# Kernel optimization log

Hardware: AMD Instinct MI355X
Metric: run time of the kernel (lower is better)

## Reference

```python
import jax, jax.numpy as jnp
import numpy as np

B, M, N = 2, 256, 256
K, P, Q, D = 8, 512, 512, 64
R, Pp, Qp, Dp = 128, 512, 512, 64
TEMP = float(np.sqrt(Dp))  # softmax temperature = sqrt(D')


def _xavier(key, shape):
    # xavier_uniform over last two dims (fan_in, fan_out), matching torch init on (K, d, D)
    fan_in, fan_out = shape[-2], shape[-1]
    lim = float(np.sqrt(6.0 / (fan_in + fan_out)))
    return jax.random.uniform(key, shape, jnp.float32, -lim, lim)


def setup_inputs() -> dict:
    key = jax.random.key(0)
    ks = jax.random.split(key, 9)
    return {
        "z": jax.random.normal(ks[0], (B, M, N, R), jnp.float32),
        "y_q": jax.random.normal(ks[1], (B, N, Qp), jnp.float32),
        "x_k": jax.random.normal(ks[2], (B, M, Pp), jnp.float32),
        "Theta_x": _xavier(ks[3], (K, P, D)),
        "Theta_y": _xavier(ks[4], (K, Q, D)),
        "Lam_x": _xavier(ks[5], (K, Pp, Dp)),
        "Lam_y": _xavier(ks[6], (K, Qp, Dp)),
        "Lam_zx": _xavier(ks[7], (K, R, Dp)),
        "Lam_zy": _xavier(ks[8], (K, R, Dp)),
    }


def reference(z, y_q, x_k, Theta_x, Theta_y, Lam_x, Lam_y, Lam_zx, Lam_zy):
    # --- mixed attention scores ---
    xt = jnp.einsum('bmp,kpd->bkmd', x_k, Lam_x)          # [B,K,M,D']
    yt = jnp.einsum('bnq,kqd->bknd', y_q, Lam_y)          # [B,K,N,D']
    r = jnp.einsum('bkmd,bknd->bkmn', xt, yt)             # pairwise term
    zy = jnp.einsum('bmnr,krd->bkmnd', z, Lam_zy)         # [B,K,M,N,D'] (large)
    r = r + jnp.einsum('bkmnd,bkmd->bkmn', zy, xt)
    r = r + jnp.einsum('bknd,bmnr,krd->bkmn', yt, z, Lam_zx)
    # --- generalised convolution (mask=None, bias=False) ---
    a = jax.nn.softmax(r / TEMP, axis=-2)                 # softmax over M (column-wise)
    xv = jnp.einsum('bmp,kpd->bkmd', x_k, Theta_x)        # value projection
    y = jnp.einsum('bkmn,bkmd,kqd->bnq', a, xv, Theta_y)  # [B,N,Q]
    return y
```

## Files before the change

kernel.cpp:

```cpp
#include <hip/hip_runtime.h>
#include <hip/hip_bf16.h>

#define LOG2E_OVER_T 0.18033688011112042f

typedef __attribute__((ext_vector_type(8))) short short8;
typedef __attribute__((ext_vector_type(4))) float f32x4;
typedef unsigned short ushort_t;
typedef unsigned long long ull_t;

#define MFMA16(a, b, c) __builtin_amdgcn_mfma_f32_16x16x32_bf16(a, b, c, 0, 0, 0)

__device__ __forceinline__ ushort_t f2bf(float f) {
    union { float f; unsigned u; } v; v.f = f;
    unsigned r = (v.u + 0x7fffu + ((v.u >> 16) & 1u)) >> 16;
    return (ushort_t)r;
}

__device__ __forceinline__ void mfma_core64(
    const ushort_t* __restrict__ Ag, int lda,
    const ushort_t* __restrict__ Btg, int ldb,
    int ksteps, f32x4 acc[2][2])
{
    __shared__ __align__(16) ushort_t As[64 * 40];
    __shared__ __align__(16) ushort_t Bs[64 * 40];
    const int t = threadIdx.x;
    const int srow = t >> 2, skc = (t & 3) * 8;
    const int lane = t & 63, w = t >> 6;
    const int wr = w >> 1, wc = w & 1;
    const int fr = lane & 15, kg = lane >> 4;
    const int aoff = (wr * 32 + fr) * 40 + kg * 8;
    const int boff = (wc * 32 + fr) * 40 + kg * 8;
    const long arow = (long)srow * lda + skc;
    const long brow = (long)srow * ldb + skc;

    short8 ra = *(const short8*)(Ag + arow);
    short8 rb = *(const short8*)(Btg + brow);
    for (int kt = 0; kt < ksteps; kt++) {
        __syncthreads();
        *(short8*)&As[srow * 40 + skc] = ra;
        *(short8*)&Bs[srow * 40 + skc] = rb;
        __syncthreads();
        if (kt + 1 < ksteps) {
            ra = *(const short8*)(Ag + arow + (kt + 1) * 32);
            rb = *(const short8*)(Btg + brow + (kt + 1) * 32);
        }
        short8 a0 = *(const short8*)&As[aoff];
        short8 a1 = *(const short8*)&As[aoff + 16 * 40];
        short8 b0 = *(const short8*)&Bs[boff];
        short8 b1 = *(const short8*)&Bs[boff + 16 * 40];
        acc[0][0] = MFMA16(a0, b0, acc[0][0]);
        acc[0][1] = MFMA16(a0, b1, acc[0][1]);
        acc[1][0] = MFMA16(a1, b0, acc[1][0]);
        acc[1][1] = MFMA16(a1, b1, acc[1][1]);
    }
}

__device__ __forceinline__ void zero_acc(f32x4 acc[2][2]) {
    const f32x4 z4 = {0.f, 0.f, 0.f, 0.f};
    acc[0][0] = z4; acc[0][1] = z4; acc[1][0] = z4; acc[1][1] = z4;
}

__global__ __launch_bounds__(256)
void convert_kernel(const float* __restrict__ x_k, const float* __restrict__ y_q,
                    const float* __restrict__ Lam_x, const float* __restrict__ Theta_x,
                    const float* __restrict__ Lam_y, const float* __restrict__ Lam_zy,
                    const float* __restrict__ Lam_zx, const float* __restrict__ Theta_y,
                    ushort_t* __restrict__ xkb, ushort_t* __restrict__ yqb,
                    ushort_t* __restrict__ WxTb, ushort_t* __restrict__ WyTb,
                    ushort_t* __restrict__ Zyb, ushort_t* __restrict__ Zxb,
                    ushort_t* __restrict__ TyTb)
{
    int i = blockIdx.x * 256 + threadIdx.x;
    if (i < 262144) { xkb[i] = f2bf(x_k[i]); return; }
    i -= 262144;
    if (i < 262144) { yqb[i] = f2bf(y_q[i]); return; }
    i -= 262144;
    if (i < 524288) {
        const int k = i >> 16, rem = i & 65535, dc = rem >> 9, p = i & 511;
        const float v = (dc < 64) ? Lam_x[((long)k * 512 + p) * 64 + dc]
                                  : Theta_x[((long)k * 512 + p) * 64 + dc - 64];
        WxTb[i] = f2bf(v); return;
    }
    i -= 524288;
    if (i < 262144) {
        const int k = i >> 15, d = (i >> 9) & 63, p = i & 511;
        WyTb[i] = f2bf(Lam_y[((long)k * 512 + p) * 64 + d]); return;
    }
    i -= 262144;
    if (i < 65536) { Zyb[i] = f2bf(Lam_zy[i]); return; }
    i -= 65536;
    if (i < 65536) { Zxb[i] = f2bf(Lam_zx[i]); return; }
    i -= 65536;
    {
        const int q = i >> 9, kd = i & 511, k = kd >> 6, d = kd & 63;
        TyTb[i] = f2bf(Theta_y[((long)k * 512 + q) * 64 + d]);
    }
}

__global__ __launch_bounds__(256)
void proj_kernel(const ushort_t* __restrict__ xkb, const ushort_t* __restrict__ yqb,
                 const ushort_t* __restrict__ WxTb, const ushort_t* __restrict__ WyTb,
                 ushort_t* __restrict__ xtb, ushort_t* __restrict__ ytb,
                 ushort_t* __restrict__ xvTb)
{
    const int side = blockIdx.z;
    const int bx = blockIdx.x, by = blockIdx.y;
    if (side == 1 && bx >= 8) return;
    f32x4 acc[2][2]; zero_acc(acc);
    const int t = threadIdx.x, lane = t & 63, w = t >> 6;
    const int wr = w >> 1, wc = w & 1, fr = lane & 15, kg = lane >> 4;

    if (side == 0) {
        mfma_core64(xkb + (long)(by * 64) * 512, 512,
                    WxTb + (long)(bx * 64) * 512, 512, 16, acc);
        const int k = bx >> 1, isxv = bx & 1;
        #pragma unroll
        for (int mi = 0; mi < 2; mi++)
        #pragma unroll
        for (int ni = 0; ni < 2; ni++) {
            const int grow0 = by * 64 + wr * 32 + mi * 16 + kg * 4;
            const int b = grow0 >> 8, m0 = grow0 & 255;
            const int d = wc * 32 + ni * 16 + fr;
            if (!isxv) {
                #pragma unroll
                for (int j = 0; j < 4; j++)
                    xtb[(((long)(b * 8 + k)) * 256 + m0 + j) * 64 + d] = f2bf(acc[mi][ni][j]);
            } else {
                ull_t pk = (ull_t)f2bf(acc[mi][ni][0])
                         | ((ull_t)f2bf(acc[mi][ni][1]) << 16)
                         | ((ull_t)f2bf(acc[mi][ni][2]) << 32)
                         | ((ull_t)f2bf(acc[mi][ni][3]) << 48);
                *(ull_t*)&xvTb[(((long)(b * 8 + k)) * 64 + d) * 256 + m0] = pk;
            }
        }
    } else {
        mfma_core64(yqb + (long)(by * 64) * 512, 512,
                    WyTb + (long)(bx * 64) * 512, 512, 16, acc);
        const int k = bx;
        #pragma unroll
        for (int mi = 0; mi < 2; mi++)
        #pragma unroll
        for (int ni = 0; ni < 2; ni++)
        #pragma unroll
        for (int j = 0; j < 4; j++) {
            const int grow = by * 64 + wr * 32 + mi * 16 + kg * 4 + j;
            const int b = grow >> 8, n = grow & 255;
            const int d = wc * 32 + ni * 16 + fr;
            ytb[(((long)(b * 8 + k)) * 256 + n) * 64 + d] = f2bf(acc[mi][ni][j]);
        }
    }
}

__global__ __launch_bounds__(256)
void step2_kernel(const ushort_t* __restrict__ xtb, const ushort_t* __restrict__ ytb,
                  const ushort_t* __restrict__ Zyb, const ushort_t* __restrict__ Zxb,
                  float* __restrict__ wzy, float* __restrict__ wzx,
                  float* __restrict__ rbuf)
{
    const int bz = blockIdx.x;
    const ushort_t *Ag, *Btg;
    float* C; int ldc; long coff;
    if (bz < 256) {
        const int which = bz >> 7, idx = bz & 127;
        const int bk = idx >> 3, tile = idx & 7, mt = tile >> 1, nt = tile & 1;
        const int k = bk & 7;
        Ag = (which ? ytb : xtb) + ((long)bk * 256 + mt * 64) * 64;
        Btg = (which ? Zxb : Zyb) + ((long)k * 128 + nt * 64) * 64;
        C = which ? wzx : wzy; ldc = 128;
        coff = ((long)bk * 256 + mt * 64) * 128 + nt * 64;
    } else {
        const int idx = bz - 256;
        const int bk = idx >> 4, tile = idx & 15, mt = tile >> 2, nt = tile & 3;
        Ag = xtb + ((long)bk * 256 + mt * 64) * 64;
        Btg = ytb + ((long)bk * 256 + nt * 64) * 64;
        C = rbuf; ldc = 256;
        coff = ((long)bk * 256 + mt * 64) * 256 + nt * 64;
    }
    f32x4 acc[2][2]; zero_acc(acc);
    mfma_core64(Ag, 64, Btg, 64, 2, acc);
    const int t = threadIdx.x, lane = t & 63, w = t >> 6;
    const int wr = w >> 1, wc = w & 1, fr = lane & 15, kg = lane >> 4;
    #pragma unroll
    for (int mi = 0; mi < 2; mi++)
    #pragma unroll
    for (int ni = 0; ni < 2; ni++)
    #pragma unroll
    for (int j = 0; j < 4; j++)
        C[coff + (long)(wr * 32 + mi * 16 + kg * 4 + j) * ldc + wc * 32 + ni * 16 + fr]
            = acc[mi][ni][j];
}

__global__ __launch_bounds__(256)
void pass1_kernel(const float* __restrict__ z, const float* __restrict__ wzy,
                  float* __restrict__ rbuf)
{
    const int m = blockIdx.x, b = blockIdx.y;
    __shared__ __align__(16) float zs[64 * 128];
    __shared__ __align__(16) float ws[8 * 128];
    const int tid = threadIdx.x;
    {
        const int k = tid >> 5, r4 = tid & 31;
        *(float4*)&ws[k * 128 + r4 * 4] =
            *(const float4*)&wzy[(((long)b * 8 + k) * 256 + m) * 128 + r4 * 4];
    }
    const int k = tid >> 5, nl = tid & 31;
    const int sw = nl & 7;
    __syncthreads();
    for (int n0 = 0; n0 < 256; n0 += 64) {
        if (n0) __syncthreads();
        const float4* zg = (const float4*)(z + (((long)b * 256 + m) * 256 + n0) * 128);
        #pragma unroll
        for (int it = 0; it < 8; it++) {
            const int idx = it * 256 + tid;
            const int nn = idx >> 5, r4 = idx & 31;
            ((float4*)zs)[nn * 32 + (r4 ^ (nn & 7))] = zg[idx];
        }
        __syncthreads();
        float acc0 = 0.f, acc1 = 0.f;
        #pragma unroll 4
        for (int r4 = 0; r4 < 32; r4++) {
            const float4 wv = ((const float4*)ws)[k * 32 + r4];
            const float4 z0 = ((const float4*)zs)[nl * 32 + (r4 ^ sw)];
            const float4 z1 = ((const float4*)zs)[(nl + 32) * 32 + (r4 ^ sw)];
            acc0 += z0.x * wv.x + z0.y * wv.y + z0.z * wv.z + z0.w * wv.w;
            acc1 += z1.x * wv.x + z1.y * wv.y + z1.z * wv.z + z1.w * wv.w;
        }
        float* rp = rbuf + (((long)b * 8 + k) * 256 + m) * 256 + n0 + nl;
        rp[0]  += acc0;
        rp[32] += acc1;
    }
}

__global__ __launch_bounds__(256)
void pass2_kernel(const float* __restrict__ z, const float* __restrict__ wzx,
                  float* __restrict__ rbufT)
{
    const int n = blockIdx.x, b = blockIdx.y;
    __shared__ __align__(16) float zs[64 * 128];
    __shared__ __align__(16) float ws[8 * 128];
    const int tid = threadIdx.x;
    {
        const int k = tid >> 5, r4 = tid & 31;
        *(float4*)&ws[k * 128 + r4 * 4] =
            *(const float4*)&wzx[(((long)b * 8 + k) * 256 + n) * 128 + r4 * 4];
    }
    const int k = tid >> 5, ml = tid & 31;
    const int sw = ml & 7;
    __syncthreads();
    for (int m0 = 0; m0 < 256; m0 += 64) {
        if (m0) __syncthreads();
        #pragma unroll
        for (int it = 0; it < 8; it++) {
            const int idx = it * 256 + tid;
            const int mm = idx >> 5, r4 = idx & 31;
            ((float4*)zs)[mm * 32 + (r4 ^ (mm & 7))] =
                *(const float4*)(z + (((long)b * 256 + m0 + mm) * 256 + n) * 128 + r4 * 4);
        }
        __syncthreads();
        float acc0 = 0.f, acc1 = 0.f;
        #pragma unroll 4
        for (int r4 = 0; r4 < 32; r4++) {
            const float4 wv = ((const float4*)ws)[k * 32 + r4];
            const float4 z0 = ((const float4*)zs)[ml * 32 + (r4 ^ sw)];
            const float4 z1 = ((const float4*)zs)[(ml + 32) * 32 + (r4 ^ sw)];
            acc0 += z0.x * wv.x + z0.y * wv.y + z0.z * wv.z + z0.w * wv.w;
            acc1 += z1.x * wv.x + z1.y * wv.y + z1.z * wv.z + z1.w * wv.w;
        }
        float* rp = rbufT + (((long)b * 8 + k) * 256 + n) * 256 + m0 + ml;
        rp[0]  = acc0;
        rp[32] = acc1;
    }
}

__global__ __launch_bounds__(256)
void softmax_combine(const float* __restrict__ rbuf, const float* __restrict__ rbufT,
                     ushort_t* __restrict__ Et, float* __restrict__ ssum)
{
    const int bk = blockIdx.x;
    const int n0 = blockIdx.y * 16;
    const int tid = threadIdx.x;
    __shared__ float S[256][17];
    __shared__ __align__(16) float T[16][260];
    __shared__ float red[16][17];
    const float* rb = rbuf + (long)bk * 65536;
    const float* rt = rbufT + (long)bk * 65536;
    {
        const int nn = tid & 15, mg = tid >> 4;
        #pragma unroll 4
        for (int i = 0; i < 16; i++) {
            const int m = mg * 16 + i;
            S[m][nn] = rb[(long)m * 256 + n0 + nn];
        }
    }
    {
        const int m4 = tid & 63, nq = tid >> 6;
        #pragma unroll
        for (int j = 0; j < 4; j++) {
            const int nn = nq * 4 + j;
            *(float4*)&T[nn][m4 * 4] = *(const float4*)&rt[(long)(n0 + nn) * 256 + m4 * 4];
        }
    }
    __syncthreads();
    const int nn = tid & 15, mg = tid >> 4;
    float loc = 0.f;
    ushort_t ebuf[16];
    #pragma unroll
    for (int i = 0; i < 16; i++) {
        const int m = mg * 16 + i;
        const float e = exp2f((S[m][nn] + T[nn][m]) * LOG2E_OVER_T);
        ebuf[i] = f2bf(e);
        loc += e;
    }
    ushort_t* ep = Et + ((long)bk * 256 + n0 + nn) * 256 + mg * 16;
    *(short8*)(ep)     = *(short8*)&ebuf[0];
    *(short8*)(ep + 8) = *(short8*)&ebuf[8];
    red[mg][nn] = loc;
    __syncthreads();
    if (tid < 16) {
        float s2 = 0.f;
        #pragma unroll
        for (int g = 0; g < 16; g++) s2 += red[g][tid];
        ssum[bk * 256 + n0 + tid] = s2;
    }
}

__global__ __launch_bounds__(256)
void ogemm_kernel(const ushort_t* __restrict__ Et, const ushort_t* __restrict__ xvTb,
                  const float* __restrict__ ssum, ushort_t* __restrict__ o2b)
{
    const int mt = blockIdx.x, bk = blockIdx.y;
    f32x4 acc[2][2]; zero_acc(acc);
    mfma_core64(Et + ((long)bk * 256 + mt * 64) * 256, 256,
                xvTb + (long)bk * 64 * 256, 256, 8, acc);
    const int t = threadIdx.x, lane = t & 63, w = t >> 6;
    const int wr = w >> 1, wc = w & 1, fr = lane & 15, kg = lane >> 4;
    const int b = bk >> 3, k = bk & 7;
    #pragma unroll
    for (int mi = 0; mi < 2; mi++)
    #pragma unroll
    for (int j = 0; j < 4; j++) {
        const int n = mt * 64 + wr * 32 + mi * 16 + kg * 4 + j;
        const float inv = 1.0f / ssum[bk * 256 + n];
        #pragma unroll
        for (int ni = 0; ni < 2; ni++) {
            const int d = wc * 32 + ni * 16 + fr;
            o2b[((long)b * 256 + n) * 512 + k * 64 + d] = f2bf(acc[mi][ni][j] * inv);
        }
    }
}

__global__ __launch_bounds__(256)
void ygemm_kernel(const ushort_t* __restrict__ o2b, const ushort_t* __restrict__ TyTb,
                  float* __restrict__ out)
{
    const int qt = blockIdx.x, mt = blockIdx.y, b = blockIdx.z;
    f32x4 acc[2][2]; zero_acc(acc);
    mfma_core64(o2b + ((long)b * 256 + mt * 64) * 512, 512,
                TyTb + (long)qt * 64 * 512, 512, 16, acc);
    const int t = threadIdx.x, lane = t & 63, w = t >> 6;
    const int wr = w >> 1, wc = w & 1, fr = lane & 15, kg = lane >> 4;
    #pragma unroll
    for (int mi = 0; mi < 2; mi++)
    #pragma unroll
    for (int ni = 0; ni < 2; ni++)
    #pragma unroll
    for (int j = 0; j < 4; j++) {
        const int n = mt * 64 + wr * 32 + mi * 16 + kg * 4 + j;
        const int q = qt * 64 + wc * 32 + ni * 16 + fr;
        out[((long)b * 256 + n) * 512 + q] = acc[mi][ni][j];
    }
}

extern "C" void kernel_launch(void* const* d_in, const int* in_sizes, int n_in,
                              void* d_out, int out_size, void* d_ws, size_t ws_size,
                              hipStream_t stream)
{
    const float* z       = (const float*)d_in[0];
    const float* y_q     = (const float*)d_in[1];
    const float* x_k     = (const float*)d_in[2];
    const float* Theta_x = (const float*)d_in[3];
    const float* Theta_y = (const float*)d_in[4];
    const float* Lam_x   = (const float*)d_in[5];
    const float* Lam_y   = (const float*)d_in[6];
    const float* Lam_zx  = (const float*)d_in[7];
    const float* Lam_zy  = (const float*)d_in[8];
    float* out = (float*)d_out;

    float*    ws   = (float*)d_ws;
    ushort_t* U    = (ushort_t*)d_ws;
    float*    rbufT = ws;
    ushort_t* WxTb  = U;
    ushort_t* WyTb  = U + 524288;
    ushort_t* Zyb   = U + 786432;
    ushort_t* Zxb   = U + 851968;
    ushort_t* xkb   = U + 917504;
    ushort_t* yqb   = U + 1179648;
    float*    rbuf  = ws + 1048576;
    float*    wzy   = ws + 2097152;
    ushort_t* Et    = U + 4194304;
    float*    wzx   = ws + 2621440;
    ushort_t* xtb   = U + 6291456;
    ushort_t* o2b   = xtb;
    ushort_t* ytb   = U + 6553600;
    float*    ssum  = ws + 3276800;
    ushort_t* xvTb  = U + 6815744;
    ushort_t* TyTb  = U + 7077888;

    convert_kernel<<<6656, 256, 0, stream>>>(x_k, y_q, Lam_x, Theta_x, Lam_y,
        Lam_zy, Lam_zx, Theta_y, xkb, yqb, WxTb, WyTb, Zyb, Zxb, TyTb);

    proj_kernel<<<dim3(16, 8, 2), 256, 0, stream>>>(xkb, yqb, WxTb, WyTb,
        xtb, ytb, xvTb);

    step2_kernel<<<512, 256, 0, stream>>>(xtb, ytb, Zyb, Zxb, wzy, wzx, rbuf);

    pass1_kernel<<<dim3(256, 2), 256, 0, stream>>>(z, wzy, rbuf);

    pass2_kernel<<<dim3(256, 2), 256, 0, stream>>>(z, wzx, rbufT);

    softmax_combine<<<dim3(16, 16), 256, 0, stream>>>(rbuf, rbufT, Et, ssum);

    ogemm_kernel<<<dim3(4, 16), 256, 0, stream>>>(Et, xvTb, ssum, o2b);

    ygemm_kernel<<<dim3(8, 4, 2), 256, 0, stream>>>(o2b, TyTb, out);
}
```

Before: 73.55 us.

## Fuse score passes and softmax into one MFMA kernel with split-bf16 z

Replaces the separate pass1, pass2 and softmax_combine kernels, and the x·y pairwise GEMM, with one fused_score kernel. It computes the pairwise term and both z-contractions per 8x16 (m,n) tile using bf16 MFMAs, with z split into hi/lo bf16 parts to keep precision, then exponentiates and atomically accumulates column sums. This removes the fp32 rbuf/rbufT round trips and two launches, and lets z be read in a single kernel. The cost is z being read twice (once per contraction), an extra MFMA per hi/lo split, atomics on ssum (zeroed in convert_kernel), and bf16 intermediates for wzy/wzx.

```diff
diff --git a/kernel.cpp b/kernel.cpp
--- a/kernel.cpp
+++ b/kernel.cpp
@@ -14,6 +14,26 @@
     union { float f; unsigned u; } v; v.f = f;
     unsigned r = (v.u + 0x7fffu + ((v.u >> 16) & 1u)) >> 16;
     return (ushort_t)r;
+}
+
+__device__ __forceinline__ void split8(const float4 a, const float4 b,
+                                       short8& hi, short8& lo)
+{
+    union { float f[8]; unsigned u[8]; } Z;
+    Z.f[0] = a.x; Z.f[1] = a.y; Z.f[2] = a.z; Z.f[3] = a.w;
+    Z.f[4] = b.x; Z.f[5] = b.y; Z.f[6] = b.z; Z.f[7] = b.w;
+    union { unsigned u[4]; short8 s; } H, L;
+    #pragma unroll
+    for (int i = 0; i < 4; i++) {
+        const unsigned u0 = Z.u[2 * i], u1 = Z.u[2 * i + 1];
+        H.u[i] = __builtin_amdgcn_perm(u1, u0, 0x07060302u);
+        union { unsigned u; float f; } h0, h1;
+        h0.u = u0 & 0xffff0000u; h1.u = u1 & 0xffff0000u;
+        union { float f; unsigned u; } l0, l1;
+        l0.f = Z.f[2 * i] - h0.f; l1.f = Z.f[2 * i + 1] - h1.f;
+        L.u[i] = __builtin_amdgcn_perm(l1.u, l0.u, 0x07060302u);
+    }
+    hi = H.s; lo = L.s;
 }
 
 __device__ __forceinline__ void mfma_core64(
@@ -68,7 +88,7 @@
                     ushort_t* __restrict__ xkb, ushort_t* __restrict__ yqb,
                     ushort_t* __restrict__ WxTb, ushort_t* __restrict__ WyTb,
                     ushort_t* __restrict__ Zyb, ushort_t* __restrict__ Zxb,
-                    ushort_t* __restrict__ TyTb)
+                    ushort_t* __restrict__ TyTb, float* __restrict__ ssum)
 {
     int i = blockIdx.x * 256 + threadIdx.x;
     if (i < 262144) { xkb[i] = f2bf(x_k[i]); return; }
@@ -91,10 +111,12 @@
     i -= 65536;
     if (i < 65536) { Zxb[i] = f2bf(Lam_zx[i]); return; }
     i -= 65536;
-    {
+    if (i < 262144) {
         const int q = i >> 9, kd = i & 511, k = kd >> 6, d = kd & 63;
-        TyTb[i] = f2bf(Theta_y[((long)k * 512 + q) * 64 + d]);
-    }
+        TyTb[i] = f2bf(Theta_y[((long)k * 512 + q) * 64 + d]); return;
+    }
+    i -= 262144;
+    ssum[i] = 0.f;
 }
 
 __global__ __launch_bounds__(256)
@@ -154,28 +176,16 @@
 __global__ __launch_bounds__(256)
 void step2_kernel(const ushort_t* __restrict__ xtb, const ushort_t* __restrict__ ytb,
                   const ushort_t* __restrict__ Zyb, const ushort_t* __restrict__ Zxb,
-                  float* __restrict__ wzy, float* __restrict__ wzx,
-                  float* __restrict__ rbuf)
+                  ushort_t* __restrict__ wzyb, ushort_t* __restrict__ wzxb)
 {
     const int bz = blockIdx.x;
-    const ushort_t *Ag, *Btg;
-    float* C; int ldc; long coff;
-    if (bz < 256) {
-        const int which = bz >> 7, idx = bz & 127;
-        const int bk = idx >> 3, tile = idx & 7, mt = tile >> 1, nt = tile & 1;
-        const int k = bk & 7;
-        Ag = (which ? ytb : xtb) + ((long)bk * 256 + mt * 64) * 64;
-        Btg = (which ? Zxb : Zyb) + ((long)k * 128 + nt * 64) * 64;
-        C = which ? wzx : wzy; ldc = 128;
-        coff = ((long)bk * 256 + mt * 64) * 128 + nt * 64;
-    } else {
-        const int idx = bz - 256;
-        const int bk = idx >> 4, tile = idx & 15, mt = tile >> 2, nt = tile & 3;
-        Ag = xtb + ((long)bk * 256 + mt * 64) * 64;
-        Btg = ytb + ((long)bk * 256 + nt * 64) * 64;
-        C = rbuf; ldc = 256;
-        coff = ((long)bk * 256 + mt * 64) * 256 + nt * 64;
-    }
+    const int which = bz >> 7, idx = bz & 127;
+    const int bk = idx >> 3, tile = idx & 7, mt = tile >> 1, nt = tile & 1;
+    const int k = bk & 7;
+    const ushort_t* Ag  = (which ? ytb : xtb) + ((long)bk * 256 + mt * 64) * 64;
+    const ushort_t* Btg = (which ? Zxb : Zyb) + ((long)k * 128 + nt * 64) * 64;
+    ushort_t* C = which ? wzxb : wzyb;
+    const long coff = ((long)bk * 256 + mt * 64) * 128 + nt * 64;
     f32x4 acc[2][2]; zero_acc(acc);
     mfma_core64(Ag, 64, Btg, 64, 2, acc);
     const int t = threadIdx.x, lane = t & 63, w = t >> 6;
@@ -186,141 +196,112 @@
     for (int ni = 0; ni < 2; ni++)
     #pragma unroll
     for (int j = 0; j < 4; j++)
-        C[coff + (long)(wr * 32 + mi * 16 + kg * 4 + j) * ldc + wc * 32 + ni * 16 + fr]
-            = acc[mi][ni][j];
-}
-
-__global__ __launch_bounds__(256)
-void pass1_kernel(const float* __restrict__ z, const float* __restrict__ wzy,
-                  float* __restrict__ rbuf)
-{
-    const int m = blockIdx.x, b = blockIdx.y;
-    __shared__ __align__(16) float zs[64 * 128];
-    __shared__ __align__(16) float ws[8 * 128];
-    const int tid = threadIdx.x;
+        C[coff + (long)(wr * 32 + mi * 16 + kg * 4 + j) * 128 + wc * 32 + ni * 16 + fr]
+            = f2bf(acc[mi][ni][j]);
+}
+
+__global__ __launch_bounds__(256, 4)
+void fused_score(const float* __restrict__ z,
+                 const ushort_t* __restrict__ xtb, const ushort_t* __restrict__ ytb,
+                 const ushort_t* __restrict__ wzyb, const ushort_t* __restrict__ wzxb,
+                 ushort_t* __restrict__ Et, float* __restrict__ ssum)
+{
+    const int nt = blockIdx.x, mt = blockIdx.y, b = blockIdx.z;
+    const int m0 = mt * 8, n0 = nt * 16;
+    __shared__ float sc[8 * 8 * 17];
+    const int t = threadIdx.x, lane = t & 63, w = t >> 6;
+    const int fr = lane & 15, kg = lane >> 4;
+    const int f8 = fr & 7;
+
     {
-        const int k = tid >> 5, r4 = tid & 31;
-        *(float4*)&ws[k * 128 + r4 * 4] =
-            *(const float4*)&wzy[(((long)b * 8 + k) * 256 + m) * 128 + r4 * 4];
-    }
-    const int k = tid >> 5, nl = tid & 31;
-    const int sw = nl & 7;
+        const long ybase = ((long)(b * 8) * 256 + n0 + fr) * 64 + kg * 8;
+        const long xbase = ((long)(b * 8) * 256 + m0 + f8) * 64 + kg * 8;
+        #pragma unroll
+        for (int kk = 0; kk < 2; kk++) {
+            const int k = w * 2 + kk;
+            const long ko = (long)k * 256 * 64;
+            f32x4 acc = {0.f, 0.f, 0.f, 0.f};
+            #pragma unroll
+            for (int s = 0; s < 2; s++) {
+                short8 av = *(const short8*)(ytb + ybase + ko + s * 32);
+                short8 bv = *(const short8*)(xtb + xbase + ko + s * 32);
+                acc = MFMA16(av, bv, acc);
+            }
+            if (fr < 8) {
+                #pragma unroll
+                for (int j = 0; j < 4; j++)
+                    sc[k * 136 + fr * 17 + kg * 4 + j] = acc[j];
+            }
+        }
+    }
     __syncthreads();
-    for (int n0 = 0; n0 < 256; n0 += 64) {
-        if (n0) __syncthreads();
-        const float4* zg = (const float4*)(z + (((long)b * 256 + m) * 256 + n0) * 128);
-        #pragma unroll
-        for (int it = 0; it < 8; it++) {
-            const int idx = it * 256 + tid;
-            const int nn = idx >> 5, r4 = idx & 31;
-            ((float4*)zs)[nn * 32 + (r4 ^ (nn & 7))] = zg[idx];
-        }
-        __syncthreads();
-        float acc0 = 0.f, acc1 = 0.f;
-        #pragma unroll 4
-        for (int r4 = 0; r4 < 32; r4++) {
-            const float4 wv = ((const float4*)ws)[k * 32 + r4];
-            const float4 z0 = ((const float4*)zs)[nl * 32 + (r4 ^ sw)];
-            const float4 z1 = ((const float4*)zs)[(nl + 32) * 32 + (r4 ^ sw)];
-            acc0 += z0.x * wv.x + z0.y * wv.y + z0.z * wv.z + z0.w * wv.w;
-            acc1 += z1.x * wv.x + z1.y * wv.y + z1.z * wv.z + z1.w * wv.w;
-        }
-        float* rp = rbuf + (((long)b * 8 + k) * 256 + m) * 256 + n0 + nl;
-        rp[0]  += acc0;
-        rp[32] += acc1;
-    }
-}
-
-__global__ __launch_bounds__(256)
-void pass2_kernel(const float* __restrict__ z, const float* __restrict__ wzx,
-                  float* __restrict__ rbufT)
-{
-    const int n = blockIdx.x, b = blockIdx.y;
-    __shared__ __align__(16) float zs[64 * 128];
-    __shared__ __align__(16) float ws[8 * 128];
-    const int tid = threadIdx.x;
+
     {
-        const int k = tid >> 5, r4 = tid & 31;
-        *(float4*)&ws[k * 128 + r4 * 4] =
-            *(const float4*)&wzx[(((long)b * 8 + k) * 256 + n) * 128 + r4 * 4];
-    }
-    const int k = tid >> 5, ml = tid & 31;
-    const int sw = ml & 7;
+        #pragma unroll
+        for (int mi = 0; mi < 2; mi++) {
+            const int ml = w * 2 + mi;
+            const int m = m0 + ml;
+            const float* zr = z + (((long)b * 256 + m) * 256 + n0 + fr) * 128 + kg * 8;
+            const ushort_t* wp = wzyb + (((long)b * 8 + f8) * 256 + m) * 128 + kg * 8;
+            f32x4 acc = {0.f, 0.f, 0.f, 0.f};
+            #pragma unroll
+            for (int s = 0; s < 4; s++) {
+                float4 z0 = *(const float4*)(zr + s * 32);
+                float4 z1 = *(const float4*)(zr + s * 32 + 4);
+                short8 wv = *(const short8*)(wp + s * 32);
+                short8 hi, lo;
+                split8(z0, z1, hi, lo);
+                acc = MFMA16(hi, wv, acc);
+                acc = MFMA16(lo, wv, acc);
+            }
+            if (fr < 8) {
+                #pragma unroll
+                for (int j = 0; j < 4; j++)
+                    sc[fr * 136 + ml * 17 + kg * 4 + j] += acc[j];
+            }
+        }
+    }
     __syncthreads();
-    for (int m0 = 0; m0 < 256; m0 += 64) {
-        if (m0) __syncthreads();
-        #pragma unroll
-        for (int it = 0; it < 8; it++) {
-            const int idx = it * 256 + tid;
-            const int mm = idx >> 5, r4 = idx & 31;
-            ((float4*)zs)[mm * 32 + (r4 ^ (mm & 7))] =
-                *(const float4*)(z + (((long)b * 256 + m0 + mm) * 256 + n) * 128 + r4 * 4);
-        }
-        __syncthreads();
-        float acc0 = 0.f, acc1 = 0.f;
-        #pragma unroll 4
-        for (int r4 = 0; r4 < 32; r4++) {
-            const float4 wv = ((const float4*)ws)[k * 32 + r4];
-            const float4 z0 = ((const float4*)zs)[ml * 32 + (r4 ^ sw)];
-            const float4 z1 = ((const float4*)zs)[(ml + 32) * 32 + (r4 ^ sw)];
-            acc0 += z0.x * wv.x + z0.y * wv.y + z0.z * wv.z + z0.w * wv.w;
-            acc1 += z1.x * wv.x + z1.y * wv.y + z1.z * wv.z + z1.w * wv.w;
-        }
-        float* rp = rbufT + (((long)b * 8 + k) * 256 + n) * 256 + m0 + ml;
-        rp[0]  = acc0;
-        rp[32] = acc1;
-    }
-}
-
-__global__ __launch_bounds__(256)
-void softmax_combine(const float* __restrict__ rbuf, const float* __restrict__ rbufT,
-                     ushort_t* __restrict__ Et, float* __restrict__ ssum)
-{
-    const int bk = blockIdx.x;
-    const int n0 = blockIdx.y * 16;
-    const int tid = threadIdx.x;
-    __shared__ float S[256][17];
-    __shared__ __align__(16) float T[16][260];
-    __shared__ float red[16][17];
-    const float* rb = rbuf + (long)bk * 65536;
-    const float* rt = rbufT + (long)bk * 65536;
+
     {
-        const int nn = tid & 15, mg = tid >> 4;
-        #pragma unroll 4
-        for (int i = 0; i < 16; i++) {
-            const int m = mg * 16 + i;
-            S[m][nn] = rb[(long)m * 256 + n0 + nn];
-        }
-    }
-    {
-        const int m4 = tid & 63, nq = tid >> 6;
-        #pragma unroll
-        for (int j = 0; j < 4; j++) {
-            const int nn = nq * 4 + j;
-            *(float4*)&T[nn][m4 * 4] = *(const float4*)&rt[(long)(n0 + nn) * 256 + m4 * 4];
+        #pragma unroll
+        for (int ni = 0; ni < 4; ni++) {
+            const int nl = w * 4 + ni;
+            const int n = n0 + nl;
+            const float* zr = z + (((long)b * 256 + m0 + f8) * 256 + n) * 128 + kg * 8;
+            const ushort_t* wp = wzxb + (((long)b * 8 + f8) * 256 + n) * 128 + kg * 8;
+            f32x4 acc = {0.f, 0.f, 0.f, 0.f};
+            #pragma unroll
+            for (int s = 0; s < 4; s++) {
+                float4 z0 = *(const float4*)(zr + s * 32);
+                float4 z1 = *(const float4*)(zr + s * 32 + 4);
+                short8 wv = *(const short8*)(wp + s * 32);
+                short8 hi, lo;
+                split8(z0, z1, hi, lo);
+                acc = MFMA16(hi, wv, acc);
+                acc = MFMA16(lo, wv, acc);
+            }
+            if (fr < 8 && kg < 2) {
+                #pragma unroll
+                for (int j = 0; j < 4; j++)
+                    sc[fr * 136 + (kg * 4 + j) * 17 + nl] += acc[j];
+            }
         }
     }
     __syncthreads();
-    const int nn = tid & 15, mg = tid >> 4;
-    float loc = 0.f;
-    ushort_t ebuf[16];
-    #pragma unroll
-    for (int i = 0; i < 16; i++) {
-        const int m = mg * 16 + i;
-        const float e = exp2f((S[m][nn] + T[nn][m]) * LOG2E_OVER_T);
-        ebuf[i] = f2bf(e);
-        loc += e;
-    }
-    ushort_t* ep = Et + ((long)bk * 256 + n0 + nn) * 256 + mg * 16;
-    *(short8*)(ep)     = *(short8*)&ebuf[0];
-    *(short8*)(ep + 8) = *(short8*)&ebuf[8];
-    red[mg][nn] = loc;
-    __syncthreads();
-    if (tid < 16) {
-        float s2 = 0.f;
-        #pragma unroll
-        for (int g = 0; g < 16; g++) s2 += red[g][tid];
-        ssum[bk * 256 + n0 + tid] = s2;
+
+    if (t < 128) {
+        const int k = t >> 4, nl = t & 15;
+        float sum = 0.f;
+        ushort_t eb[8];
+        #pragma unroll
+        for (int j = 0; j < 8; j++) {
+            const float e = exp2f(sc[k * 136 + j * 17 + nl] * LOG2E_OVER_T);
+            eb[j] = f2bf(e);
+            sum += e;
+        }
+        *(short8*)(Et + (((long)b * 8 + k) * 256 + n0 + nl) * 256 + m0) = *(short8*)eb;
+        atomicAdd(&ssum[(b * 8 + k) * 256 + n0 + nl], sum);
     }
 }
 
@@ -386,39 +367,33 @@
     const float* Lam_zy  = (const float*)d_in[8];
     float* out = (float*)d_out;
 
-    float*    ws   = (float*)d_ws;
-    ushort_t* U    = (ushort_t*)d_ws;
-    float*    rbufT = ws;
-    ushort_t* WxTb  = U;
-    ushort_t* WyTb  = U + 524288;
-    ushort_t* Zyb   = U + 786432;
-    ushort_t* Zxb   = U + 851968;
-    ushort_t* xkb   = U + 917504;
-    ushort_t* yqb   = U + 1179648;
-    float*    rbuf  = ws + 1048576;
-    float*    wzy   = ws + 2097152;
-    ushort_t* Et    = U + 4194304;
-    float*    wzx   = ws + 2621440;
-    ushort_t* xtb   = U + 6291456;
-    ushort_t* o2b   = xtb;
-    ushort_t* ytb   = U + 6553600;
-    float*    ssum  = ws + 3276800;
-    ushort_t* xvTb  = U + 6815744;
-    ushort_t* TyTb  = U + 7077888;
-
-    convert_kernel<<<6656, 256, 0, stream>>>(x_k, y_q, Lam_x, Theta_x, Lam_y,
-        Lam_zy, Lam_zx, Theta_y, xkb, yqb, WxTb, WyTb, Zyb, Zxb, TyTb);
+    ushort_t* U = (ushort_t*)d_ws;
+    ushort_t* xkb  = U;
+    ushort_t* yqb  = U + 262144;
+    ushort_t* WxTb = U + 524288;
+    ushort_t* WyTb = U + 1048576;
+    ushort_t* Zyb  = U + 1310720;
+    ushort_t* Zxb  = U + 1376256;
+    ushort_t* TyTb = U + 1441792;
+    ushort_t* xtb  = U + 1703936;
+    ushort_t* ytb  = U + 1966080;
+    ushort_t* xvTb = U + 2228224;
+    ushort_t* wzyb = U + 2490368;
+    ushort_t* wzxb = U + 3014656;
+    ushort_t* Et   = U + 3538944;
+    ushort_t* o2b  = U + 4587520;
+    float*    ssum = (float*)(U + 4849664);
+
+    convert_kernel<<<6672, 256, 0, stream>>>(x_k, y_q, Lam_x, Theta_x, Lam_y,
+        Lam_zy, Lam_zx, Theta_y, xkb, yqb, WxTb, WyTb, Zyb, Zxb, TyTb, ssum);
 
     proj_kernel<<<dim3(16, 8, 2), 256, 0, stream>>>(xkb, yqb, WxTb, WyTb,
         xtb, ytb, xvTb);
 
-    step2_kernel<<<512, 256, 0, stream>>>(xtb, ytb, Zyb, Zxb, wzy, wzx, rbuf);
-
-    pass1_kernel<<<dim3(256, 2), 256, 0, stream>>>(z, wzy, rbuf);
-
-    pass2_kernel<<<dim3(256, 2), 256, 0, stream>>>(z, wzx, rbufT);
-
-    softmax_combine<<<dim3(16, 16), 256, 0, stream>>>(rbuf, rbufT, Et, ssum);
+    step2_kernel<<<256, 256, 0, stream>>>(xtb, ytb, Zyb, Zxb, wzyb, wzxb);
+
+    fused_score<<<dim3(16, 32, 2), 256, 0, stream>>>(z, xtb, ytb, wzyb, wzxb,
+        Et, ssum);
 
     ogemm_kernel<<<dim3(4, 16), 256, 0, stream>>>(Et, xvTb, ssum, o2b);
 
```

Result: faster. 71.05 us (-3.4%).

## Fuse softmax exponent and row-sum into the z pass2 kernel, drop combine kernel

Applied to the files above, without the earlier changes.

Removes the separate softmax_combine kernel. The second z-streaming pass now adds the partial scores and computes exp2, writing bf16 exponents and per-column sums through a warp shuffle reduction. The wzy/wzx intermediates are now stored in bf16 with a [b,m,k,r] layout so each block can load its weights contiguously. The pairwise term is written transposed as t1 and folded in by passB. This saves one launch and a full fp32 read/write round trip of the score buffer. The cost is scattered, strided SB reads and 2-byte Et stores in passC, plus extra bf16 rounding of the weights.

```diff
diff --git a/kernel.cpp b/kernel.cpp
--- a/kernel.cpp
+++ b/kernel.cpp
@@ -14,6 +14,11 @@
     union { float f; unsigned u; } v; v.f = f;
     unsigned r = (v.u + 0x7fffu + ((v.u >> 16) & 1u)) >> 16;
     return (ushort_t)r;
+}
+
+__device__ __forceinline__ float bf2f(ushort_t u) {
+    union { unsigned u; float f; } v; v.u = (unsigned)u << 16;
+    return v.f;
 }
 
 __device__ __forceinline__ void mfma_core64(
@@ -154,54 +159,64 @@
 __global__ __launch_bounds__(256)
 void step2_kernel(const ushort_t* __restrict__ xtb, const ushort_t* __restrict__ ytb,
                   const ushort_t* __restrict__ Zyb, const ushort_t* __restrict__ Zxb,
-                  float* __restrict__ wzy, float* __restrict__ wzx,
-                  float* __restrict__ rbuf)
+                  ushort_t* __restrict__ wzyb, ushort_t* __restrict__ wzxb,
+                  float* __restrict__ t1)
 {
     const int bz = blockIdx.x;
-    const ushort_t *Ag, *Btg;
-    float* C; int ldc; long coff;
+    const int t = threadIdx.x, lane = t & 63, w = t >> 6;
+    const int wr = w >> 1, wc = w & 1, fr = lane & 15, kg = lane >> 4;
+
     if (bz < 256) {
         const int which = bz >> 7, idx = bz & 127;
         const int bk = idx >> 3, tile = idx & 7, mt = tile >> 1, nt = tile & 1;
-        const int k = bk & 7;
-        Ag = (which ? ytb : xtb) + ((long)bk * 256 + mt * 64) * 64;
-        Btg = (which ? Zxb : Zyb) + ((long)k * 128 + nt * 64) * 64;
-        C = which ? wzx : wzy; ldc = 128;
-        coff = ((long)bk * 256 + mt * 64) * 128 + nt * 64;
+        const int k = bk & 7, b = bk >> 3;
+        const ushort_t* Ag  = (which ? ytb : xtb) + ((long)bk * 256 + mt * 64) * 64;
+        const ushort_t* Btg = (which ? Zxb : Zyb) + ((long)k * 128 + nt * 64) * 64;
+        ushort_t* C = which ? wzxb : wzyb;
+        f32x4 acc[2][2]; zero_acc(acc);
+        mfma_core64(Ag, 64, Btg, 64, 2, acc);
+        #pragma unroll
+        for (int mi = 0; mi < 2; mi++)
+        #pragma unroll
+        for (int ni = 0; ni < 2; ni++)
+        #pragma unroll
+        for (int j = 0; j < 4; j++) {
+            const int m_glob = mt * 64 + wr * 32 + mi * 16 + kg * 4 + j;
+            const int r_glob = nt * 64 + wc * 32 + ni * 16 + fr;
+            C[(((long)b * 256 + m_glob) * 8 + k) * 128 + r_glob] = f2bf(acc[mi][ni][j]);
+        }
     } else {
         const int idx = bz - 256;
-        const int bk = idx >> 4, tile = idx & 15, mt = tile >> 2, nt = tile & 3;
-        Ag = xtb + ((long)bk * 256 + mt * 64) * 64;
-        Btg = ytb + ((long)bk * 256 + nt * 64) * 64;
-        C = rbuf; ldc = 256;
-        coff = ((long)bk * 256 + mt * 64) * 256 + nt * 64;
-    }
-    f32x4 acc[2][2]; zero_acc(acc);
-    mfma_core64(Ag, 64, Btg, 64, 2, acc);
-    const int t = threadIdx.x, lane = t & 63, w = t >> 6;
-    const int wr = w >> 1, wc = w & 1, fr = lane & 15, kg = lane >> 4;
-    #pragma unroll
-    for (int mi = 0; mi < 2; mi++)
-    #pragma unroll
-    for (int ni = 0; ni < 2; ni++)
-    #pragma unroll
-    for (int j = 0; j < 4; j++)
-        C[coff + (long)(wr * 32 + mi * 16 + kg * 4 + j) * ldc + wc * 32 + ni * 16 + fr]
-            = acc[mi][ni][j];
-}
-
-__global__ __launch_bounds__(256)
-void pass1_kernel(const float* __restrict__ z, const float* __restrict__ wzy,
-                  float* __restrict__ rbuf)
+        const int bk = idx >> 4, tile = idx & 15, nt2 = tile >> 2, mt2 = tile & 3;
+        f32x4 acc[2][2]; zero_acc(acc);
+        mfma_core64(ytb + ((long)bk * 256 + nt2 * 64) * 64, 64,
+                    xtb + ((long)bk * 256 + mt2 * 64) * 64, 64, 2, acc);
+        #pragma unroll
+        for (int mi = 0; mi < 2; mi++)
+        #pragma unroll
+        for (int ni = 0; ni < 2; ni++)
+        #pragma unroll
+        for (int j = 0; j < 4; j++) {
+            const int n_glob = nt2 * 64 + wr * 32 + mi * 16 + kg * 4 + j;
+            const int m_glob = mt2 * 64 + wc * 32 + ni * 16 + fr;
+            t1[((long)bk * 256 + m_glob) * 256 + n_glob] = acc[mi][ni][j];
+        }
+    }
+}
+
+__global__ __launch_bounds__(256)
+void passB_kernel(const float* __restrict__ z, const ushort_t* __restrict__ wzyb,
+                  const float* __restrict__ t1, float* __restrict__ SB)
 {
     const int m = blockIdx.x, b = blockIdx.y;
     __shared__ __align__(16) float zs[64 * 128];
     __shared__ __align__(16) float ws[8 * 128];
     const int tid = threadIdx.x;
     {
-        const int k = tid >> 5, r4 = tid & 31;
-        *(float4*)&ws[k * 128 + r4 * 4] =
-            *(const float4*)&wzy[(((long)b * 8 + k) * 256 + m) * 128 + r4 * 4];
+        const ushort_t* wp = wzyb + ((long)b * 256 + m) * 1024;
+        #pragma unroll
+        for (int j = 0; j < 4; j++)
+            ws[tid * 4 + j] = bf2f(wp[tid * 4 + j]);
     }
     const int k = tid >> 5, nl = tid & 31;
     const int sw = nl & 7;
@@ -225,27 +240,30 @@
             acc0 += z0.x * wv.x + z0.y * wv.y + z0.z * wv.z + z0.w * wv.w;
             acc1 += z1.x * wv.x + z1.y * wv.y + z1.z * wv.z + z1.w * wv.w;
         }
-        float* rp = rbuf + (((long)b * 8 + k) * 256 + m) * 256 + n0 + nl;
-        rp[0]  += acc0;
-        rp[32] += acc1;
-    }
-}
-
-__global__ __launch_bounds__(256)
-void pass2_kernel(const float* __restrict__ z, const float* __restrict__ wzx,
-                  float* __restrict__ rbufT)
+        const long base = ((long)(b * 8 + k) * 256 + m) * 256 + n0 + nl;
+        SB[base]      = acc0 + t1[base];
+        SB[base + 32] = acc1 + t1[base + 32];
+    }
+}
+
+__global__ __launch_bounds__(256)
+void passC_kernel(const float* __restrict__ z, const ushort_t* __restrict__ wzxb,
+                  const float* __restrict__ SB, ushort_t* __restrict__ Et,
+                  float* __restrict__ ssum)
 {
     const int n = blockIdx.x, b = blockIdx.y;
     __shared__ __align__(16) float zs[64 * 128];
     __shared__ __align__(16) float ws[8 * 128];
     const int tid = threadIdx.x;
     {
-        const int k = tid >> 5, r4 = tid & 31;
-        *(float4*)&ws[k * 128 + r4 * 4] =
-            *(const float4*)&wzx[(((long)b * 8 + k) * 256 + n) * 128 + r4 * 4];
+        const ushort_t* wp = wzxb + ((long)b * 256 + n) * 1024;
+        #pragma unroll
+        for (int j = 0; j < 4; j++)
+            ws[tid * 4 + j] = bf2f(wp[tid * 4 + j]);
     }
     const int k = tid >> 5, ml = tid & 31;
     const int sw = ml & 7;
+    float ksum = 0.f;
     __syncthreads();
     for (int m0 = 0; m0 < 256; m0 += 64) {
         if (m0) __syncthreads();
@@ -266,62 +284,21 @@
             acc0 += z0.x * wv.x + z0.y * wv.y + z0.z * wv.z + z0.w * wv.w;
             acc1 += z1.x * wv.x + z1.y * wv.y + z1.z * wv.z + z1.w * wv.w;
         }
-        float* rp = rbufT + (((long)b * 8 + k) * 256 + n) * 256 + m0 + ml;
-        rp[0]  = acc0;
-        rp[32] = acc1;
-    }
-}
-
-__global__ __launch_bounds__(256)
-void softmax_combine(const float* __restrict__ rbuf, const float* __restrict__ rbufT,
-                     ushort_t* __restrict__ Et, float* __restrict__ ssum)
-{
-    const int bk = blockIdx.x;
-    const int n0 = blockIdx.y * 16;
-    const int tid = threadIdx.x;
-    __shared__ float S[256][17];
-    __shared__ __align__(16) float T[16][260];
-    __shared__ float red[16][17];
-    const float* rb = rbuf + (long)bk * 65536;
-    const float* rt = rbufT + (long)bk * 65536;
-    {
-        const int nn = tid & 15, mg = tid >> 4;
-        #pragma unroll 4
-        for (int i = 0; i < 16; i++) {
-            const int m = mg * 16 + i;
-            S[m][nn] = rb[(long)m * 256 + n0 + nn];
-        }
-    }
-    {
-        const int m4 = tid & 63, nq = tid >> 6;
-        #pragma unroll
-        for (int j = 0; j < 4; j++) {
-            const int nn = nq * 4 + j;
-            *(float4*)&T[nn][m4 * 4] = *(const float4*)&rt[(long)(n0 + nn) * 256 + m4 * 4];
-        }
-    }
-    __syncthreads();
-    const int nn = tid & 15, mg = tid >> 4;
-    float loc = 0.f;
-    ushort_t ebuf[16];
-    #pragma unroll
-    for (int i = 0; i < 16; i++) {
-        const int m = mg * 16 + i;
-        const float e = exp2f((S[m][nn] + T[nn][m]) * LOG2E_OVER_T);
-        ebuf[i] = f2bf(e);
-        loc += e;
-    }
-    ushort_t* ep = Et + ((long)bk * 256 + n0 + nn) * 256 + mg * 16;
-    *(short8*)(ep)     = *(short8*)&ebuf[0];
-    *(short8*)(ep + 8) = *(short8*)&ebuf[8];
-    red[mg][nn] = loc;
-    __syncthreads();
-    if (tid < 16) {
-        float s2 = 0.f;
-        #pragma unroll
-        for (int g = 0; g < 16; g++) s2 += red[g][tid];
-        ssum[bk * 256 + n0 + tid] = s2;
-    }
+        const long sbase = ((long)(b * 8 + k) * 256 + m0 + ml) * 256 + n;
+        const float s0v = acc0 + SB[sbase];
+        const float s1v = acc1 + SB[sbase + 32 * 256];
+        const float e0 = exp2f(s0v * LOG2E_OVER_T);
+        const float e1 = exp2f(s1v * LOG2E_OVER_T);
+        const long ebase = ((long)(b * 8 + k) * 256 + n) * 256 + m0 + ml;
+        Et[ebase]      = f2bf(e0);
+        Et[ebase + 32] = f2bf(e1);
+        ksum += e0 + e1;
+    }
+    #pragma unroll
+    for (int off = 16; off >= 1; off >>= 1)
+        ksum += __shfl_xor(ksum, off);
+    if (ml == 0)
+        ssum[(b * 8 + k) * 256 + n] = ksum;
 }
 
 __global__ __launch_bounds__(256)
@@ -386,25 +363,24 @@
     const float* Lam_zy  = (const float*)d_in[8];
     float* out = (float*)d_out;
 
-    float*    ws   = (float*)d_ws;
-    ushort_t* U    = (ushort_t*)d_ws;
-    float*    rbufT = ws;
-    ushort_t* WxTb  = U;
-    ushort_t* WyTb  = U + 524288;
-    ushort_t* Zyb   = U + 786432;
-    ushort_t* Zxb   = U + 851968;
-    ushort_t* xkb   = U + 917504;
-    ushort_t* yqb   = U + 1179648;
-    float*    rbuf  = ws + 1048576;
-    float*    wzy   = ws + 2097152;
-    ushort_t* Et    = U + 4194304;
-    float*    wzx   = ws + 2621440;
-    ushort_t* xtb   = U + 6291456;
-    ushort_t* o2b   = xtb;
-    ushort_t* ytb   = U + 6553600;
-    float*    ssum  = ws + 3276800;
-    ushort_t* xvTb  = U + 6815744;
-    ushort_t* TyTb  = U + 7077888;
+    ushort_t* U = (ushort_t*)d_ws;
+    ushort_t* xkb  = U;
+    ushort_t* yqb  = U + 262144;
+    ushort_t* WxTb = U + 524288;
+    ushort_t* WyTb = U + 1048576;
+    ushort_t* Zyb  = U + 1310720;
+    ushort_t* Zxb  = U + 1376256;
+    float*    SB   = (float*)U;
+    ushort_t* TyTb = U + 2097152;
+    ushort_t* xtb  = U + 2359296;
+    ushort_t* ytb  = U + 2621440;
+    ushort_t* xvTb = U + 2883584;
+    ushort_t* wzyb = U + 3145728;
+    ushort_t* wzxb = U + 3670016;
+    ushort_t* Et   = U + 4194304;
+    ushort_t* o2b  = U + 5242880;
+    float*    ssum = (float*)(U + 5505024);
+    float*    t1   = (float*)(U + 5513216);
 
     convert_kernel<<<6656, 256, 0, stream>>>(x_k, y_q, Lam_x, Theta_x, Lam_y,
         Lam_zy, Lam_zx, Theta_y, xkb, yqb, WxTb, WyTb, Zyb, Zxb, TyTb);
@@ -412,13 +388,11 @@
     proj_kernel<<<dim3(16, 8, 2), 256, 0, stream>>>(xkb, yqb, WxTb, WyTb,
         xtb, ytb, xvTb);
 
-    step2_kernel<<<512, 256, 0, stream>>>(xtb, ytb, Zyb, Zxb, wzy, wzx, rbuf);
-
-    pass1_kernel<<<dim3(256, 2), 256, 0, stream>>>(z, wzy, rbuf);
-
-    pass2_kernel<<<dim3(256, 2), 256, 0, stream>>>(z, wzx, rbufT);
-
-    softmax_combine<<<dim3(16, 16), 256, 0, stream>>>(rbuf, rbufT, Et, ssum);
+    step2_kernel<<<512, 256, 0, stream>>>(xtb, ytb, Zyb, Zxb, wzyb, wzxb, t1);
+
+    passB_kernel<<<dim3(256, 2), 256, 0, stream>>>(z, wzyb, t1, SB);
+
+    passC_kernel<<<dim3(256, 2), 256, 0, stream>>>(z, wzxb, SB, Et, ssum);
 
     ogemm_kernel<<<dim3(4, 16), 256, 0, stream>>>(Et, xvTb, ssum, o2b);
 
```

Result: faster. 70.32 us (-4.4%).
